# Kernel tuning notes

Hardware: AMD Instinct MI355X
Metric: run time of the kernel (lower is better)

Reference implementation:

```python
import jax, jax.numpy as jnp
import numpy as np

N = 50000   # nodes
E = 1600000 # edges
G = 512     # graphs in batch
IN_DIM, EMBED, H, D = 64, 128, 4, 32
D1, D2, D3 = 128, 64, 16
NEG_SLOPE = 0.2  # DGL GATConv default


def setup_inputs() -> dict:
    key = jax.random.key(0)
    ks = jax.random.split(key, 16)
    def glorot(k, shape):
        fan = shape[0] + shape[-1]
        return jax.random.normal(k, shape, jnp.float32) * jnp.sqrt(2.0 / fan)
    return {
        "feature": jax.random.normal(ks[0], (N, IN_DIM), jnp.float32),
        "src": jax.random.randint(ks[1], (E,), 0, N, jnp.int32),
        "dst": jax.random.randint(ks[2], (E,), 0, N, jnp.int32),
        "graph_ids": jnp.sort(jax.random.randint(ks[3], (N,), 0, G, jnp.int32)),
        "W0": glorot(ks[4], (IN_DIM, EMBED)), "b0": jnp.zeros((EMBED,), jnp.float32),
        "Wfc": glorot(ks[5], (EMBED, H * D)),
        "attn_l": glorot(ks[6], (H, D)), "attn_r": glorot(ks[7], (H, D)),
        "gat_bias": jnp.zeros((H * D,), jnp.float32),
        "W1": glorot(ks[8], (H * D, D1)), "b1": jnp.zeros((D1,), jnp.float32),
        "W2": glorot(ks[9], (D1, D2)), "b2": jnp.zeros((D2,), jnp.float32),
        "W3": glorot(ks[10], (D2, D3)), "b3": jnp.zeros((D3,), jnp.float32),
    }


def reference(feature, src, dst, graph_ids, W0, b0, Wfc, attn_l, attn_r,
              gat_bias, W1, b1, W2, b2, W3, b3):
    # initial dense embed
    h = feature @ W0 + b0                                   # [N, EMBED]
    # GATConv
    feat = (h @ Wfc).reshape(N, H, D)                       # [N,H,D]
    el = jnp.einsum('nhd,hd->nh', feat, attn_l)             # [N,H]
    er = jnp.einsum('nhd,hd->nh', feat, attn_r)
    e = jax.nn.leaky_relu(el[src] + er[dst], NEG_SLOPE)     # [E,H]
    # segment softmax over incoming edges of each dst node
    m = jax.ops.segment_max(e, dst, num_segments=N)         # [N,H]
    ex = jnp.exp(e - m[dst])                                # [E,H]
    denom = jax.ops.segment_sum(ex, dst, num_segments=N)    # [N,H]
    a = ex / denom[dst]                                     # [E,H]
    msg = a[:, :, None] * feat[src]                         # [E,H,D]
    rst = jax.ops.segment_sum(msg, dst, num_segments=N)     # [N,H,D]
    rst = rst + gat_bias.reshape(1, H, D)
    hn = rst.reshape(N, H * D)
    # AvgPooling per graph
    sums = jax.ops.segment_sum(hn, graph_ids, num_segments=G)           # [G,H*D]
    cnts = jax.ops.segment_sum(jnp.ones((N,), hn.dtype), graph_ids, num_segments=G)
    hg = sums / jnp.maximum(cnts, 1.0)[:, None]
    # dense head
    out = jax.nn.elu(hg)
    out = jax.nn.elu(out @ W1 + b1)
    out = jax.nn.elu(out @ W2 + b2)
    out = out @ W3 + b3                                     # [G, D3]
    atten = a[:, :, None]                                   # [E,H,1] like DGL
    return out, atten
```

## Files before the change

kernel.cpp:

```cpp
#include <hip/hip_runtime.h>
#include <hip/hip_fp16.h>
#include <math.h>

#define N_NODES 50000
#define E_EDGES 1600000
#define G_GRAPHS 512
#define IN_DIM 64
#define EMBED 128
#define HD 128
#define NHEAD 4
#define D1 128
#define D2 64
#define D3 16
#define NEG_SLOPE 0.2f
#define NB ((N_NODES + 127) >> 7)
#define HT_TILE 4096
#define HT_BLOCKS ((E_EDGES + HT_TILE - 1) / HT_TILE)
#define PT_TILE 8192
#define PT_BLOCKS ((E_EDGES + PT_TILE - 1) / PT_TILE)
#define K1_TILES ((N_NODES + 63) / 64)
#define FB_CAP 8192
#define M2_EDGE_BLK ((E_EDGES + 2047) / 2048)
#define K6_HALF 6250

typedef float vfloat4 __attribute__((ext_vector_type(4)));
typedef float vfloat2 __attribute__((ext_vector_type(2)));
typedef unsigned short ushort_t;

static __device__ __forceinline__ float leaky(float x) { return x > 0.f ? x : NEG_SLOPE * x; }

__global__ void __launch_bounds__(256) k0hg(const int* __restrict__ dst, int* __restrict__ ghist,
                                            const float* __restrict__ W0, const float* __restrict__ b0,
                                            const float* __restrict__ Wfc, float* __restrict__ Wc,
                                            float* __restrict__ bc) {
    __shared__ int lh[4][NB];
    const int t = threadIdx.x;
    if (blockIdx.x < HT_BLOCKS) {
        const int wid = t >> 6;
        for (int i = t; i < NB; i += 256) {
            lh[0][i] = 0; lh[1][i] = 0; lh[2][i] = 0; lh[3][i] = 0;
        }
        __syncthreads();
        const long e0 = (long)blockIdx.x * HT_TILE;
#pragma unroll
        for (int k = 0; k < HT_TILE / 256; ++k) {
            long e = e0 + t + k * 256;
            if (e < E_EDGES) atomicAdd(&lh[wid][dst[e] >> 7], 1);
        }
        __syncthreads();
        for (int i = t; i < NB; i += 256) {
            int v = lh[0][i] + lh[1][i] + lh[2][i] + lh[3][i];
            if (v) atomicAdd(&ghist[i], v);
        }
    } else {
        int tid = (int)(blockIdx.x - HT_BLOCKS) * 256 + t;
        if (tid < IN_DIM * HD) {
            int i = tid >> 7, j = tid & 127;
            float acc = 0.f;
            for (int k = 0; k < EMBED; ++k) acc += W0[i * EMBED + k] * Wfc[k * HD + j];
            Wc[tid] = acc;
        } else if (tid < IN_DIM * HD + HD) {
            int j = tid - IN_DIM * HD;
            float acc = 0.f;
            for (int k = 0; k < EMBED; ++k) acc += b0[k] * Wfc[k * HD + j];
            bc[j] = acc;
        }
    }
}

#define SMEM_BYTES 53248
__global__ void __launch_bounds__(256) k1pt(
    const float* __restrict__ A, const float* __restrict__ W,
    const float* __restrict__ b, const float* __restrict__ attn_l,
    const float* __restrict__ attn_r,
    const int* __restrict__ src, const int* __restrict__ dst,
    const int* __restrict__ ghist, int* __restrict__ cursor0,
    unsigned char* __restrict__ feat, float* __restrict__ el,
    float* __restrict__ er, unsigned int* __restrict__ part) {
    __shared__ __align__(16) char smem[SMEM_BYTES];
    const int t = threadIdx.x;
    if (blockIdx.x < K1_TILES) {
        float* Ws = (float*)smem;
        float(*As)[68] = (float(*)[68])(smem + 32768);
        const int cc = t & 31, rt = t >> 5;
        const int c0 = cc * 4, r0 = rt * 8;
        const int row0 = (int)blockIdx.x * 64;
        {
            const float4* Wg = (const float4*)W;
            float4* Wl = (float4*)Ws;
#pragma unroll
            for (int j = 0; j < (IN_DIM * HD / 4) / 256; ++j) Wl[t + j * 256] = Wg[t + j * 256];
        }
#pragma unroll
        for (int j = 0; j < 4; ++j) {
            int i2 = t + j * 256;
            int row = i2 >> 4, kq = i2 & 15;
            int gr = row0 + row;
            float4 v = (gr < N_NODES) ? *(const float4*)(A + (size_t)gr * IN_DIM + kq * 4)
                                      : make_float4(0.f, 0.f, 0.f, 0.f);
            *(float4*)&As[row][kq * 4] = v;
        }
        __syncthreads();
        float acc[8][4];
#pragma unroll
        for (int i = 0; i < 8; ++i)
#pragma unroll
            for (int j = 0; j < 4; ++j) acc[i][j] = 0.f;
        for (int k4 = 0; k4 < IN_DIM / 4; ++k4) {
            vfloat4 w0 = *(const vfloat4*)&Ws[(k4 * 4 + 0) * HD + c0];
            vfloat4 w1 = *(const vfloat4*)&Ws[(k4 * 4 + 1) * HD + c0];
            vfloat4 w2 = *(const vfloat4*)&Ws[(k4 * 4 + 2) * HD + c0];
            vfloat4 w3 = *(const vfloat4*)&Ws[(k4 * 4 + 3) * HD + c0];
#pragma unroll
            for (int i = 0; i < 8; ++i) {
                vfloat4 a = *(const vfloat4*)&As[r0 + i][k4 * 4];
#pragma unroll
                for (int j = 0; j < 4; ++j)
                    acc[i][j] += a.x * w0[j] + a.y * w1[j] + a.z * w2[j] + a.w * w3[j];
            }
        }
        {
            vfloat4 bcv = *(const vfloat4*)(b + c0);
#pragma unroll
            for (int i = 0; i < 8; ++i)
#pragma unroll
                for (int j = 0; j < 4; ++j) acc[i][j] += bcv[j];
        }
#pragma unroll
        for (int i = 0; i < 8; ++i) {
            int gr = row0 + r0 + i;
            if (gr < N_NODES) {
                unsigned int ww = __builtin_amdgcn_cvt_pk_fp8_f32(acc[i][0], acc[i][1], 0, false);
                ww = __builtin_amdgcn_cvt_pk_fp8_f32(acc[i][2], acc[i][3], ww, true);
                *(unsigned int*)(feat + (size_t)gr * HD + c0) = ww;
            }
        }
        {
            vfloat4 al = *(const vfloat4*)(attn_l + c0);
            vfloat4 ar = *(const vfloat4*)(attn_r + c0);
            float pl[8], pr[8];
#pragma unroll
            for (int i = 0; i < 8; ++i) {
                pl[i] = acc[i][0] * al[0] + acc[i][1] * al[1] + acc[i][2] * al[2] + acc[i][3] * al[3];
                pr[i] = acc[i][0] * ar[0] + acc[i][1] * ar[1] + acc[i][2] * ar[2] + acc[i][3] * ar[3];
            }
#pragma unroll
            for (int off = 1; off <= 4; off <<= 1) {
#pragma unroll
                for (int i = 0; i < 8; ++i) {
                    pl[i] += __shfl_xor(pl[i], off);
                    pr[i] += __shfl_xor(pr[i], off);
                }
            }
            if ((cc & 7) == 0) {
                const int h = cc >> 3;
#pragma unroll
                for (int i = 0; i < 8; ++i) {
                    int gr = row0 + r0 + i;
                    if (gr < N_NODES) {
                        el[gr * 4 + h] = pl[i];
                        er[gr * 4 + h] = pr[i];
                    }
                }
            }
        }
    } else {
        int(*hist)[NB] = (int(*)[NB])smem;
        int(*lcur)[NB] = (int(*)[NB])(smem + 6256);
        int* tot = (int*)(smem + 12512);
        int* offs = (int*)(smem + 14076);
        int* base_s = (int*)(smem + 15640);
        int* gt = (int*)(smem + 17204);
        int* offsG = (int*)(smem + 18768);
        unsigned int* stage = (unsigned int*)(smem + 20336);
        const int lane = t & 63, wid = t >> 6;
        const int tile = (int)blockIdx.x - K1_TILES;
        const long e0 = (long)tile * PT_TILE;
        const int cnt = (int)min((long)PT_TILE, (long)E_EDGES - e0);
        for (int i = t; i < NB; i += 256) {
            hist[0][i] = 0; hist[1][i] = 0; hist[2][i] = 0; hist[3][i] = 0;
            gt[i] = ghist[i];
        }
        __syncthreads();
        unsigned int v[PT_TILE / 256];
#pragma unroll
        for (int k = 0; k < PT_TILE / 256; ++k) {
            int i = t + k * 256;
            if (i < cnt) {
                int d = dst[e0 + i];
                v[k] = ((unsigned int)d << 16) | (unsigned int)src[e0 + i];
                atomicAdd(&hist[wid][d >> 7], 1);
            } else v[k] = 0xFFFFFFFFu;
        }
        __syncthreads();
        for (int i = t; i < NB; i += 256) {
            int h0 = hist[0][i], h1 = hist[1][i], h2 = hist[2][i], h3 = hist[3][i];
            hist[0][i] = 0; hist[1][i] = h0; hist[2][i] = h0 + h1; hist[3][i] = h0 + h1 + h2;
            tot[i] = h0 + h1 + h2 + h3;
        }
        __syncthreads();
        if (wid == 0) {
            int run = 0;
            for (int c = 0; c < (NB + 63) / 64; ++c) {
                int i = c * 64 + lane;
                int vv = (i < NB) ? tot[i] : 0;
                int incl = vv;
#pragma unroll
                for (int off = 1; off < 64; off <<= 1) {
                    int o = __shfl_up(incl, off, 64);
                    if (lane >= off) incl += o;
                }
                if (i < NB) offs[i] = run + incl - vv;
                run += __shfl(incl, 63, 64);
            }
        } else if (wid == 1) {
            int run = 0;
            for (int c = 0; c < (NB + 63) / 64; ++c) {
                int i = c * 64 + lane;
                int vv = (i < NB) ? gt[i] : 0;
                int incl = vv;
#pragma unroll
                for (int off = 1; off < 64; off <<= 1) {
                    int o = __shfl_up(incl, off, 64);
                    if (lane >= off) incl += o;
                }
                if (i < NB) offsG[i] = run + incl - vv;
                run += __shfl(incl, 63, 64);
            }
        }
        __syncthreads();
        for (int i = t; i < NB; i += 256) {
            int tt2 = tot[i];
            base_s[i] = offsG[i] + (tt2 ? atomicAdd(&cursor0[i], tt2) : 0);
            int ob = offs[i];
            lcur[0][i] = ob + hist[0][i];
            lcur[1][i] = ob + hist[1][i];
            lcur[2][i] = ob + hist[2][i];
            lcur[3][i] = ob + hist[3][i];
        }
        __syncthreads();
#pragma unroll
        for (int k = 0; k < PT_TILE / 256; ++k) {
            if (v[k] != 0xFFFFFFFFu) {
                int bb = v[k] >> 23;
                int pos = atomicAdd(&lcur[wid][bb], 1);
                stage[pos] = v[k];
            }
        }
        __syncthreads();
        for (int i = t; i < cnt; i += 256) {
            unsigned int p = stage[i];
            int bb = p >> 23;
            part[base_s[bb] + (i - offs[bb])] = p & 0x7FFFFFu;
        }
    }
}

__global__ void __launch_bounds__(256) fb_fill(const unsigned int* __restrict__ part,
                                               const int* __restrict__ ghist,
                                               int* __restrict__ rowstart,
                                               ushort_t* __restrict__ csr_src) {
    const int b = blockIdx.x, t = threadIdx.x, lane = t & 63, wid = t >> 6;
    __shared__ int degl[4][128], totl[128], offl[128], curl[4][128];
    __shared__ int red[4], s0s[2];
    __shared__ unsigned int lpart[FB_CAP];
    __shared__ ushort_t lsrc[FB_CAP];
    {
        int partial = 0;
        for (int i = t; i < b; i += 256) partial += ghist[i];
#pragma unroll
        for (int off = 32; off; off >>= 1) partial += __shfl_xor(partial, off);
        if (lane == 0) red[wid] = partial;
        if (t < 128) { degl[0][t] = 0; degl[1][t] = 0; degl[2][t] = 0; degl[3][t] = 0; }
        __syncthreads();
        if (t == 0) {
            int s0 = red[0] + red[1] + red[2] + red[3];
            s0s[0] = s0;
            s0s[1] = s0 + ghist[b];
        }
        __syncthreads();
    }
    const int s0 = s0s[0], s1 = s0s[1];
    const int cnt = s1 - s0;
    if (cnt <= FB_CAP) {
        for (int i = t; i < cnt; i += 256) {
            unsigned int p = part[s0 + i];
            lpart[i] = p;
            atomicAdd(&degl[wid][p >> 16], 1);
        }
    } else {
        for (int i = t; i < cnt; i += 256) {
            unsigned int p = part[s0 + i];
            atomicAdd(&degl[wid][p >> 16], 1);
        }
    }
    __syncthreads();
    if (t < 128) {
        int d0 = degl[0][t], d1 = degl[1][t], d2 = degl[2][t], d3 = degl[3][t];
        degl[0][t] = 0; degl[1][t] = d0; degl[2][t] = d0 + d1; degl[3][t] = d0 + d1 + d2;
        totl[t] = d0 + d1 + d2 + d3;
    }
    __syncthreads();
    if (wid == 0) {
        int run = 0;
        for (int c = 0; c < 2; ++c) {
            int i = c * 64 + lane;
            int vv = totl[i];
            int incl = vv;
#pragma unroll
            for (int off = 1; off < 64; off <<= 1) {
                int o = __shfl_up(incl, off, 64);
                if (lane >= off) incl += o;
            }
            offl[i] = run + incl - vv;
            run += __shfl(incl, 63, 64);
        }
    }
    __syncthreads();
    if (t < 128) {
        int ob = offl[t];
        curl[0][t] = ob + degl[0][t];
        curl[1][t] = ob + degl[1][t];
        curl[2][t] = ob + degl[2][t];
        curl[3][t] = ob + degl[3][t];
        int node = (b << 7) + t;
        if (node < N_NODES) rowstart[node] = s0 + ob;
    }
    if (b == 0 && t == 0) rowstart[N_NODES] = E_EDGES;
    __syncthreads();
    if (cnt <= FB_CAP) {
        for (int i = t; i < cnt; i += 256) {
            unsigned int p = lpart[i];
            int pos = atomicAdd(&curl[wid][p >> 16], 1);
            lsrc[pos] = (ushort_t)(p & 0xFFFFu);
        }
        __syncthreads();
        for (int i = t; i < cnt; i += 256) csr_src[s0 + i] = lsrc[i];
    } else {
        for (int i = t; i < cnt; i += 256) {
            unsigned int p = part[s0 + i];
            int pos = atomicAdd(&curl[wid][p >> 16], 1);
            csr_src[s0 + pos] = (ushort_t)(p & 0xFFFFu);
        }
    }
}

__global__ void __launch_bounds__(256) k6_aggregate(
    const ushort_t* __restrict__ csr_src, const int* __restrict__ rowstart,
    const float* __restrict__ el, const float* __restrict__ er,
    const unsigned char* __restrict__ feat, const float* __restrict__ gat_bias,
    float* __restrict__ er_rd, float* __restrict__ hn, int node_base) {
    __shared__ uint2 s_pk[4][64][4];
    const int wid = threadIdx.x >> 6;
    const int lane = threadIdx.x & 63;
    const int n = node_base + blockIdx.x * 4 + wid;
    if (n >= N_NODES) return;
    const int start = rowstart[n];
    const int end = rowstart[n + 1];
    const int deg = end - start;

    const int e0 = lane >> 2;
    const int h = lane & 3;
    const float erh = er[n * 4 + h];
    float sm = 0.f;
    for (int base = 0; base < deg; base += 16) {
        const int e = base + e0;
        if (e < deg) {
            const int s = csr_src[start + e];
            const float ex = __expf(leaky(el[s * 4 + h] + erh));
            sm += ex;
            if (e < 64)
                s_pk[wid][e][h] = make_uint2((unsigned int)s << 7, __float_as_uint(ex));
        }
    }
#pragma unroll
    for (int off = 4; off <= 32; off <<= 1) sm += __shfl_xor(sm, off);
    const float rd = sm > 0.f ? 1.f / sm : 0.f;
    if (lane < 4) {
        er_rd[(size_t)n * 8 + lane] = erh;
        er_rd[(size_t)n * 8 + 4 + lane] = rd;
    }

    const int g4 = lane >> 4, gl = lane & 15;
    const int h2 = gl >> 2;
    const float rdh = __shfl(rd, h2);
    vfloat2 acc0 = {0.f, 0.f}, acc1 = {0.f, 0.f}, acc2 = {0.f, 0.f}, acc3 = {0.f, 0.f};

    if (deg <= 64) {
        const uint2* pk = &s_pk[wid][0][h2];
        const unsigned char* fg = feat + (gl << 3);
        int idx = g4;
        for (; idx + 4 < deg; idx += 8) {
            const uint2 pA = pk[idx * 4];
            const uint2 pB = pk[(idx + 4) * 4];
            const uint2 wA = *(const uint2*)(fg + pA.x);
            const uint2 wB = *(const uint2*)(fg + pB.x);
            const float exA = __uint_as_float(pA.y);
            const float exB = __uint_as_float(pB.y);
            const vfloat2 eA = {exA, exA}, eB = {exB, exB};
            acc0 += eA * __builtin_amdgcn_cvt_pk_f32_fp8(wA.x, false);
            acc1 += eA * __builtin_amdgcn_cvt_pk_f32_fp8(wA.x, true);
            acc2 += eA * __builtin_amdgcn_cvt_pk_f32_fp8(wA.y, false);
            acc3 += eA * __builtin_amdgcn_cvt_pk_f32_fp8(wA.y, true);
            acc0 += eB * __builtin_amdgcn_cvt_pk_f32_fp8(wB.x, false);
            acc1 += eB * __builtin_amdgcn_cvt_pk_f32_fp8(wB.x, true);
            acc2 += eB * __builtin_amdgcn_cvt_pk_f32_fp8(wB.y, false);
            acc3 += eB * __builtin_amdgcn_cvt_pk_f32_fp8(wB.y, true);
        }
        if (idx < deg) {
            const uint2 p = pk[idx * 4];
            const uint2 w = *(const uint2*)(fg + p.x);
            const float ex = __uint_as_float(p.y);
            const vfloat2 ev = {ex, ex};
            acc0 += ev * __builtin_amdgcn_cvt_pk_f32_fp8(w.x, false);
            acc1 += ev * __builtin_amdgcn_cvt_pk_f32_fp8(w.x, true);
            acc2 += ev * __builtin_amdgcn_cvt_pk_f32_fp8(w.y, false);
            acc3 += ev * __builtin_amdgcn_cvt_pk_f32_fp8(w.y, true);
        }
    } else {
        const float erh2 = __shfl(erh, h2);
        const unsigned char* fg = feat + (gl << 3);
        for (int e = start + g4; e < end; e += 4) {
            const unsigned int s = csr_src[e];
            const float ex = __expf(leaky(el[s * 4 + h2] + erh2));
            const vfloat2 ev = {ex, ex};
            const uint2 w = *(const uint2*)(fg + ((size_t)s << 7));
            acc0 += ev * __builtin_amdgcn_cvt_pk_f32_fp8(w.x, false);
            acc1 += ev * __builtin_amdgcn_cvt_pk_f32_fp8(w.x, true);
            acc2 += ev * __builtin_amdgcn_cvt_pk_f32_fp8(w.y, false);
            acc3 += ev * __builtin_amdgcn_cvt_pk_f32_fp8(w.y, true);
        }
    }
    {
        const vfloat2 rv = {rdh, rdh};
        acc0 *= rv; acc1 *= rv; acc2 *= rv; acc3 *= rv;
    }
#pragma unroll
    for (int off = 16; off <= 32; off <<= 1) {
        acc0.x += __shfl_xor(acc0.x, off);
        acc0.y += __shfl_xor(acc0.y, off);
        acc1.x += __shfl_xor(acc1.x, off);
        acc1.y += __shfl_xor(acc1.y, off);
        acc2.x += __shfl_xor(acc2.x, off);
        acc2.y += __shfl_xor(acc2.y, off);
        acc3.x += __shfl_xor(acc3.x, off);
        acc3.y += __shfl_xor(acc3.y, off);
    }
    if (lane < 16) {
        const float4 b0 = ((const float4*)gat_bias)[gl * 2];
        const float4 b1 = ((const float4*)gat_bias)[gl * 2 + 1];
        float4* hp = (float4*)(hn + (size_t)n * HD + gl * 8);
        hp[0] = make_float4(acc0.x + b0.x, acc0.y + b0.y, acc1.x + b0.z, acc1.y + b0.w);
        hp[1] = make_float4(acc2.x + b1.x, acc2.y + b1.y, acc3.x + b1.z, acc3.y + b1.w);
    }
}

__global__ void __launch_bounds__(512) m2b_mlp_attn(
    const int* __restrict__ src, const int* __restrict__ dst,
    const float* __restrict__ el, const float* __restrict__ er_rd,
    const float* __restrict__ hn, const int* __restrict__ graph_ids,
    const float* __restrict__ W1, const float* __restrict__ b1,
    const float* __restrict__ W2, const float* __restrict__ b2,
    const float* __restrict__ W3, const float* __restrict__ b3,
    float* __restrict__ a_out, float* __restrict__ out) {
    const int t = threadIdx.x;
    if (blockIdx.x < G_GRAPHS) {
        const int g = (int)blockIdx.x;
        const int tt = t & 127, part = t >> 7;
        __shared__ int bounds[2];
        __shared__ double pool[4][128];
        __shared__ double x[128], y[128];
        if (t < 2) {
            const int target = g + t;
            int lo = 0, hi = N_NODES;
            while (lo < hi) {
                int mid = (lo + hi) >> 1;
                if (graph_ids[mid] < target) lo = mid + 1; else hi = mid;
            }
            bounds[t] = lo;
        }
        __syncthreads();
        const int lo = bounds[0], hi = bounds[1];
        double s = 0.0;
        for (int n = lo + part; n < hi; n += 4) s += (double)hn[(size_t)n * HD + tt];
        pool[part][tt] = s;
        __syncthreads();
        if (t < 128) {
            const double cnt = (double)(hi - lo);
            const double sum = pool[0][t] + pool[1][t] + pool[2][t] + pool[3][t];
            const double v = sum / fmax(cnt, 1.0);
            x[t] = v > 0.0 ? v : expm1(v);
        }
        __syncthreads();
        if (t < 128) {
            double acc = (double)b1[t];
            for (int k = 0; k < HD; ++k) acc += x[k] * (double)W1[k * D1 + t];
            y[t] = acc > 0.0 ? acc : expm1(acc);
        }
        __syncthreads();
        if (t < D2) {
            double a2 = (double)b2[t];
            for (int k = 0; k < D1; ++k) a2 += y[k] * (double)W2[k * D2 + t];
            x[t] = a2 > 0.0 ? a2 : expm1(a2);
        }
        __syncthreads();
        if (t < D3) {
            double a3 = (double)b3[t];
            for (int k = 0; k < D2; ++k) a3 += x[k] * (double)W3[k * D3 + t];
            out[g * D3 + t] = (float)a3;
        }
    } else {
        const long base4 = (long)(blockIdx.x - G_GRAPHS) * 2048 + (long)t * 4;
        if (base4 + 3 < E_EDGES) {
            const int4 s4 = *(const int4*)(src + base4);
            const int4 d4 = *(const int4*)(dst + base4);
            const int sx[4] = {s4.x, s4.y, s4.z, s4.w};
            const int dx[4] = {d4.x, d4.y, d4.z, d4.w};
            float4 el4[4], er4[4], r4[4];
#pragma unroll
            for (int k = 0; k < 4; ++k) {
                el4[k] = *(const float4*)(el + sx[k] * 4);
                er4[k] = *(const float4*)(er_rd + (size_t)dx[k] * 8);
                r4[k] = *(const float4*)(er_rd + (size_t)dx[k] * 8 + 4);
            }
#pragma unroll
            for (int k = 0; k < 4; ++k) {
                vfloat4 a;
                a.x = __expf(leaky(el4[k].x + er4[k].x)) * r4[k].x;
                a.y = __expf(leaky(el4[k].y + er4[k].y)) * r4[k].y;
                a.z = __expf(leaky(el4[k].z + er4[k].z)) * r4[k].z;
                a.w = __expf(leaky(el4[k].w + er4[k].w)) * r4[k].w;
                __builtin_nontemporal_store(a, (vfloat4*)a_out + (base4 + k));
            }
        } else {
            for (int k = 0; k < 4; ++k) {
                const long e = base4 + k;
                if (e < E_EDGES) {
                    const int s = src[e], d = dst[e];
                    const float4 el4 = *(const float4*)(el + s * 4);
                    const float4 er4 = *(const float4*)(er_rd + (size_t)d * 8);
                    const float4 r4 = *(const float4*)(er_rd + (size_t)d * 8 + 4);
                    vfloat4 a;
                    a.x = __expf(leaky(el4.x + er4.x)) * r4.x;
                    a.y = __expf(leaky(el4.y + er4.y)) * r4.y;
                    a.z = __expf(leaky(el4.z + er4.z)) * r4.z;
                    a.w = __expf(leaky(el4.w + er4.w)) * r4.w;
                    __builtin_nontemporal_store(a, (vfloat4*)a_out + e);
                }
            }
        }
    }
}

extern "C" void kernel_launch(void* const* d_in, const int* in_sizes, int n_in,
                              void* d_out, int out_size, void* d_ws, size_t ws_size,
                              hipStream_t stream) {
    const float* feature = (const float*)d_in[0];
    const int* src = (const int*)d_in[1];
    const int* dst = (const int*)d_in[2];
    const int* graph_ids = (const int*)d_in[3];
    const float* W0 = (const float*)d_in[4];
    const float* b0 = (const float*)d_in[5];
    const float* Wfc = (const float*)d_in[6];
    const float* attn_l = (const float*)d_in[7];
    const float* attn_r = (const float*)d_in[8];
    const float* gat_bias = (const float*)d_in[9];
    const float* W1 = (const float*)d_in[10];
    const float* b1 = (const float*)d_in[11];
    const float* W2 = (const float*)d_in[12];
    const float* b2 = (const float*)d_in[13];
    const float* W3 = (const float*)d_in[14];
    const float* b3 = (const float*)d_in[15];

    char* ws = (char*)d_ws;
    size_t off = 0;
    auto carve = [&](size_t bytes) -> void* {
        void* p = ws + off;
        off += (bytes + 255) & ~(size_t)255;
        return p;
    };
    int* ghist = (int*)carve((size_t)NB * 4);
    int* cursor0 = (int*)carve((size_t)NB * 4);
    const size_t zero_span = off;
    float* Wc = (float*)carve((size_t)IN_DIM * HD * 4);
    float* bc = (float*)carve((size_t)HD * 4);
    unsigned char* feat = (unsigned char*)carve((size_t)N_NODES * HD);
    float* el = (float*)carve((size_t)N_NODES * 4 * 4);
    float* er = (float*)carve((size_t)N_NODES * 4 * 4);
    float* er_rd = (float*)carve((size_t)N_NODES * 8 * 4);
    int* rowstart = (int*)carve((size_t)(N_NODES + 1) * 4);
    unsigned int* part = (unsigned int*)carve((size_t)E_EDGES * 4);
    ushort_t* csr_src = (ushort_t*)carve((size_t)E_EDGES * 2);
    float* hn = (float*)carve((size_t)N_NODES * HD * 4);

    float* out = (float*)d_out;
    float* a_out = out + G_GRAPHS * D3;

    (void)hipMemsetAsync(d_ws, 0, zero_span, stream);
    k0hg<<<HT_BLOCKS + 33, 256, 0, stream>>>(dst, ghist, W0, b0, Wfc, Wc, bc);
    k1pt<<<K1_TILES + PT_BLOCKS, 256, 0, stream>>>(feature, Wc, bc, attn_l, attn_r,
                                                   src, dst, ghist, cursor0,
                                                   feat, el, er, part);
    fb_fill<<<NB, 256, 0, stream>>>(part, ghist, rowstart, csr_src);
    k6_aggregate<<<K6_HALF, 256, 0, stream>>>(csr_src, rowstart, el, er, feat,
                                              gat_bias, er_rd, hn, 0);
    k6_aggregate<<<K6_HALF, 256, 0, stream>>>(csr_src, rowstart, el, er, feat,
                                              gat_bias, er_rd, hn, 25000);
    m2b_mlp_attn<<<G_GRAPHS + M2_EDGE_BLK, 512, 0, stream>>>(src, dst, el, er_rd, hn,
                                                             graph_ids, W1, b1, W2, b2,
                                                             W3, b3, a_out, out);
}
```

Before: 244.5 us.

## Merge aggregate launches, drop fb_fill LDS staging, widen edge-attention blocks

The two half-range k6_aggregate launches are merged into one launch over all nodes. fb_fill no longer stages the partition words in a 32KB shared buffer and instead re-reads them from global memory in the scatter pass, cutting LDS use so more blocks can be resident. The edge-attention part of m2b now handles 4096 edges per block, with each thread doing 8 strided coalesced edges and issuing all 8 gathers before computing. The cost is a second global read of part and more registers per thread in the edge path.

```diff
diff --git a/kernel.cpp b/kernel.cpp
--- a/kernel.cpp
+++ b/kernel.cpp
@@ -20,8 +20,8 @@
 #define PT_BLOCKS ((E_EDGES + PT_TILE - 1) / PT_TILE)
 #define K1_TILES ((N_NODES + 63) / 64)
 #define FB_CAP 8192
-#define M2_EDGE_BLK ((E_EDGES + 2047) / 2048)
-#define K6_HALF 6250
+#define M2_EDGE_BLK ((E_EDGES + 4095) / 4096)
+#define M2_FULL (E_EDGES / 4096)
 
 typedef float vfloat4 __attribute__((ext_vector_type(4)));
 typedef float vfloat2 __attribute__((ext_vector_type(2)));
@@ -263,7 +263,6 @@
     const int b = blockIdx.x, t = threadIdx.x, lane = t & 63, wid = t >> 6;
     __shared__ int degl[4][128], totl[128], offl[128], curl[4][128];
     __shared__ int red[4], s0s[2];
-    __shared__ unsigned int lpart[FB_CAP];
     __shared__ ushort_t lsrc[FB_CAP];
     {
         int partial = 0;
@@ -282,17 +281,9 @@
     }
     const int s0 = s0s[0], s1 = s0s[1];
     const int cnt = s1 - s0;
-    if (cnt <= FB_CAP) {
-        for (int i = t; i < cnt; i += 256) {
-            unsigned int p = part[s0 + i];
-            lpart[i] = p;
-            atomicAdd(&degl[wid][p >> 16], 1);
-        }
-    } else {
-        for (int i = t; i < cnt; i += 256) {
-            unsigned int p = part[s0 + i];
-            atomicAdd(&degl[wid][p >> 16], 1);
-        }
+    for (int i = t; i < cnt; i += 256) {
+        unsigned int p = part[s0 + i];
+        atomicAdd(&degl[wid][p >> 16], 1);
     }
     __syncthreads();
     if (t < 128) {
@@ -330,7 +321,7 @@
     __syncthreads();
     if (cnt <= FB_CAP) {
         for (int i = t; i < cnt; i += 256) {
-            unsigned int p = lpart[i];
+            unsigned int p = part[s0 + i];
             int pos = atomicAdd(&curl[wid][p >> 16], 1);
             lsrc[pos] = (ushort_t)(p & 0xFFFFu);
         }
@@ -349,11 +340,11 @@
     const ushort_t* __restrict__ csr_src, const int* __restrict__ rowstart,
     const float* __restrict__ el, const float* __restrict__ er,
     const unsigned char* __restrict__ feat, const float* __restrict__ gat_bias,
-    float* __restrict__ er_rd, float* __restrict__ hn, int node_base) {
+    float* __restrict__ er_rd, float* __restrict__ hn) {
     __shared__ uint2 s_pk[4][64][4];
     const int wid = threadIdx.x >> 6;
     const int lane = threadIdx.x & 63;
-    const int n = node_base + blockIdx.x * 4 + wid;
+    const int n = blockIdx.x * 4 + wid;
     if (n >= N_NODES) return;
     const int start = rowstart[n];
     const int end = rowstart[n + 1];
@@ -510,31 +501,35 @@
             out[g * D3 + t] = (float)a3;
         }
     } else {
-        const long base4 = (long)(blockIdx.x - G_GRAPHS) * 2048 + (long)t * 4;
-        if (base4 + 3 < E_EDGES) {
-            const int4 s4 = *(const int4*)(src + base4);
-            const int4 d4 = *(const int4*)(dst + base4);
-            const int sx[4] = {s4.x, s4.y, s4.z, s4.w};
-            const int dx[4] = {d4.x, d4.y, d4.z, d4.w};
-            float4 el4[4], er4[4], r4[4];
-#pragma unroll
-            for (int k = 0; k < 4; ++k) {
+        const int eb = (int)blockIdx.x - G_GRAPHS;
+        const long base = (long)eb * 4096 + t;
+        if (eb < M2_FULL) {
+            int sx[8], dx[8];
+#pragma unroll
+            for (int k = 0; k < 8; ++k) {
+                const long e = base + (long)k * 512;
+                sx[k] = src[e];
+                dx[k] = dst[e];
+            }
+            float4 el4[8], er4[8], r4[8];
+#pragma unroll
+            for (int k = 0; k < 8; ++k) {
                 el4[k] = *(const float4*)(el + sx[k] * 4);
                 er4[k] = *(const float4*)(er_rd + (size_t)dx[k] * 8);
                 r4[k] = *(const float4*)(er_rd + (size_t)dx[k] * 8 + 4);
             }
 #pragma unroll
-            for (int k = 0; k < 4; ++k) {
+            for (int k = 0; k < 8; ++k) {
                 vfloat4 a;
                 a.x = __expf(leaky(el4[k].x + er4[k].x)) * r4[k].x;
                 a.y = __expf(leaky(el4[k].y + er4[k].y)) * r4[k].y;
                 a.z = __expf(leaky(el4[k].z + er4[k].z)) * r4[k].z;
                 a.w = __expf(leaky(el4[k].w + er4[k].w)) * r4[k].w;
-                __builtin_nontemporal_store(a, (vfloat4*)a_out + (base4 + k));
+                __builtin_nontemporal_store(a, (vfloat4*)a_out + (base + (long)k * 512));
             }
         } else {
-            for (int k = 0; k < 4; ++k) {
-                const long e = base4 + k;
+            for (int k = 0; k < 8; ++k) {
+                const long e = base + (long)k * 512;
                 if (e < E_EDGES) {
                     const int s = src[e], d = dst[e];
                     const float4 el4 = *(const float4*)(el + s * 4);
@@ -602,10 +597,8 @@
                                                    src, dst, ghist, cursor0,
                                                    feat, el, er, part);
     fb_fill<<<NB, 256, 0, stream>>>(part, ghist, rowstart, csr_src);
-    k6_aggregate<<<K6_HALF, 256, 0, stream>>>(csr_src, rowstart, el, er, feat,
-                                              gat_bias, er_rd, hn, 0);
-    k6_aggregate<<<K6_HALF, 256, 0, stream>>>(csr_src, rowstart, el, er, feat,
-                                              gat_bias, er_rd, hn, 25000);
+    k6_aggregate<<<(N_NODES + 3) / 4, 256, 0, stream>>>(csr_src, rowstart, el, er, feat,
+                                                        gat_bias, er_rd, hn);
     m2b_mlp_attn<<<G_GRAPHS + M2_EDGE_BLK, 512, 0, stream>>>(src, dst, el, er_rd, hn,
                                                              graph_ids, W1, b1, W2, b2,
                                                              W3, b3, a_out, out);
```

Measured after the change: 233.3 us. 1.05x faster.
